# Performance work log

Measured on AMD Instinct MI355X. Metric: run time of the kernel, lower is better.

The kernel has to match this reference:

```python
import jax, jax.numpy as jnp
import numpy as np

B, T, C, H = 2, 2048, 1024, 16
D = C // H  # head dim = 64
EPS = 1e-5


def _layernorm(x, g, b):
    mu = jnp.mean(x, axis=-1, keepdims=True)
    var = jnp.mean((x - mu) ** 2, axis=-1, keepdims=True)
    return (x - mu) * jax.lax.rsqrt(var + EPS) * g + b


def setup_inputs() -> dict:
    key = jax.random.key(0)
    ks = jax.random.split(key, 16)
    s = 1.0 / np.sqrt(C)
    inp = {
        "x": jax.random.normal(ks[0], (B, T, C), dtype=jnp.float32),
        "Wq": jax.random.normal(ks[1], (C, C), dtype=jnp.float32) * s,
        "bq": jnp.zeros((C,), jnp.float32),
        "Wk": jax.random.normal(ks[2], (C, C), dtype=jnp.float32) * s,
        "bk": jnp.zeros((C,), jnp.float32),
        "Wv": jax.random.normal(ks[3], (C, C), dtype=jnp.float32) * s,
        "bv": jnp.zeros((C,), jnp.float32),
        "Wo": jax.random.normal(ks[4], (C, C), dtype=jnp.float32) * s,
        "bo": jnp.zeros((C,), jnp.float32),
        "ln1_g": jnp.ones((C,), jnp.float32),
        "ln1_b": jnp.zeros((C,), jnp.float32),
        "ln2_g": jnp.ones((C,), jnp.float32),
        "ln2_b": jnp.zeros((C,), jnp.float32),
        "W1": jax.random.normal(ks[5], (C, 4 * C), dtype=jnp.float32) * s,
        "b1": jnp.zeros((4 * C,), jnp.float32),
        "W2": jax.random.normal(ks[6], (4 * C, C), dtype=jnp.float32) * (1.0 / np.sqrt(4 * C)),
        "b2": jnp.zeros((C,), jnp.float32),
    }
    return inp


def _block(x, Wq, bq, Wk, bk, Wv, bv, Wo, bo, ln1_g, ln1_b, ln2_g, ln2_b, W1, b1, W2, b2):
    # --- attention sublayer (pre-LN, residual) ---
    h = _layernorm(x, ln1_g, ln1_b)
    q = (h @ Wq + bq).reshape(B, T, H, D)
    k = (h @ Wk + bk).reshape(B, T, H, D)
    v = (h @ Wv + bv).reshape(B, T, H, D)
    scores = jnp.einsum("bthd,bshd->bhts", q, k) * (1.0 / np.sqrt(D))
    attn = jax.nn.softmax(scores, axis=-1)  # dropout is identity at eval
    y = jnp.einsum("bhts,bshd->bthd", attn, v).reshape(B, T, C)
    x = x + (y @ Wo + bo)
    # --- MLP sublayer (pre-LN, residual) ---
    h2 = _layernorm(x, ln2_g, ln2_b)
    m = jax.nn.gelu(h2 @ W1 + b1, approximate=False)  # torch nn.GELU() is exact erf
    x = x + (m @ W2 + b2)
    return x


def reference(x, Wq, bq, Wk, bk, Wv, bv, Wo, bo, ln1_g, ln1_b, ln2_g, ln2_b, W1, b1, W2, b2):
    return _block(x, Wq, bq, Wk, bk, Wv, bv, Wo, bo, ln1_g, ln1_b, ln2_g, ln2_b, W1, b1, W2, b2)
```

## Files before the change

### kernel.cpp

```cpp
#include <hip/hip_runtime.h>
#include <math.h>

typedef unsigned short u16;
typedef unsigned int   u32;
using bf16x8 = __attribute__((ext_vector_type(8))) short;
using f32x4  = __attribute__((ext_vector_type(4))) float;
using f32x16 = __attribute__((ext_vector_type(16))) float;

static constexpr int Bb = 2, Tt = 2048, Cc = 1024, Hh = 16, Dd = 64;
static constexpr int QS = 3072;

__device__ __forceinline__ u16 f2bf(float f){
  u32 u = __builtin_bit_cast(u32, f);
  u += 0x7fffu + ((u >> 16) & 1u);
  return (u16)(u >> 16);
}

__device__ __forceinline__ void gl2lds16(const void* g, void* l){
  __builtin_amdgcn_global_load_lds((const __attribute__((address_space(1))) void*)g,
                                   (__attribute__((address_space(3))) void*)l, 16, 0, 0);
}

template<int N> __device__ __forceinline__ void waitvm(){
  if constexpr (N == 0) asm volatile("s_waitcnt vmcnt(0)" ::: "memory");
  else if constexpr (N == 3) asm volatile("s_waitcnt vmcnt(3)" ::: "memory");
  else if constexpr (N == 4) asm volatile("s_waitcnt vmcnt(4)" ::: "memory");
}

__device__ __forceinline__ void barrier_pin(){
  __builtin_amdgcn_s_barrier();
  __builtin_amdgcn_sched_barrier(0);
}

__device__ __forceinline__ f32x4 mfma16(bf16x8 a, bf16x8 b, f32x4 c){
  return __builtin_amdgcn_mfma_f32_16x16x32_bf16(a, b, c, 0, 0, 0);
}
__device__ __forceinline__ f32x16 mfma32(bf16x8 a, bf16x8 b, f32x16 c){
  return __builtin_amdgcn_mfma_f32_32x32x16_bf16(a, b, c, 0, 0, 0);
}

__device__ __forceinline__ float exp2f_fast(float x){
#if __has_builtin(__builtin_amdgcn_exp2f)
  return __builtin_amdgcn_exp2f(x);
#else
  return __expf(x * 0.69314718056f);
#endif
}

__device__ __forceinline__ float gelu_f(float x){
  return 0.5f * x * (1.0f + erff(x * 0.70710678118654752f));
}

__device__ __forceinline__ void plane_swap(u32& a, u32& b){
  asm("v_permlane32_swap_b32 %0, %1" : "+v"(a), "+v"(b));
}
__device__ __forceinline__ u32 cvtpk_bf16(float lo, float hi){
  u32 r;
  asm("v_cvt_pk_bf16_f32 %0, %1, %2" : "=v"(r) : "v"(lo), "v"(hi));
  return r;
}

__global__ __launch_bounds__(256) void ln_kernel(const float* __restrict__ x,
    const float* __restrict__ g, const float* __restrict__ b, u16* __restrict__ out)
{
  int row = blockIdx.x;
  int tid = threadIdx.x;
  const float4* xr = (const float4*)(x + (size_t)row * Cc);
  float4 v = xr[tid];
  float s  = v.x + v.y + v.z + v.w;
  float s2 = v.x*v.x + v.y*v.y + v.z*v.z + v.w*v.w;
  #pragma unroll
  for (int off = 1; off < 64; off <<= 1){ s += __shfl_xor(s, off); s2 += __shfl_xor(s2, off); }
  __shared__ float red[8];
  int wid = tid >> 6;
  if ((tid & 63) == 0){ red[wid] = s; red[4 + wid] = s2; }
  __syncthreads();
  s  = red[0] + red[1] + red[2] + red[3];
  s2 = red[4] + red[5] + red[6] + red[7];
  float mu   = s * (1.0f / Cc);
  float var  = s2 * (1.0f / Cc) - mu * mu;
  float rstd = rsqrtf(var + 1e-5f);
  const float4 gg = ((const float4*)g)[tid];
  const float4 bb = ((const float4*)b)[tid];
  ushort4 o;
  o.x = f2bf((v.x - mu) * rstd * gg.x + bb.x);
  o.y = f2bf((v.y - mu) * rstd * gg.y + bb.y);
  o.z = f2bf((v.z - mu) * rstd * gg.z + bb.z);
  o.w = f2bf((v.w - mu) * rstd * gg.w + bb.w);
  *(ushort4*)(out + (size_t)row * Cc + tid * 4) = o;
}

__global__ __launch_bounds__(256) void transpose_cast_kernel(const float* __restrict__ in,
    u16* __restrict__ out, int R, int Ccols)
{
  __shared__ float tile[32][33];
  int tx = threadIdx.x, ty = threadIdx.y;
  int c0 = blockIdx.x * 32, r0 = blockIdx.y * 32;
  #pragma unroll
  for (int j = 0; j < 4; j++) tile[ty + j*8][tx] = in[(size_t)(r0 + ty + j*8) * Ccols + c0 + tx];
  __syncthreads();
  #pragma unroll
  for (int j = 0; j < 4; j++) out[(size_t)(c0 + ty + j*8) * R + r0 + tx] = f2bf(tile[tx][ty + j*8]);
}

__global__ __launch_bounds__(256) void pack3_kernel(const float* __restrict__ a,
    const float* __restrict__ b, const float* __restrict__ c, float* __restrict__ o)
{
  int i = blockIdx.x * 256 + threadIdx.x;
  float v = (i < 1024) ? a[i] : (i < 2048 ? b[i - 1024] : c[i - 2048]);
  o[i] = v;
}

__global__ __launch_bounds__(256) void transpose_v_kernel(const u16* __restrict__ v, u16* __restrict__ vt)
{
  __shared__ u16 tile[32][33];
  int tx = threadIdx.x, ty = threadIdx.y;
  int bh = blockIdx.z; int b = bh >> 4, h = bh & 15;
  int t0 = blockIdx.x * 32, d0 = blockIdx.y * 32;
  const u16* src = v + (size_t)b * Tt * QS + h * Dd;
  #pragma unroll
  for (int j = 0; j < 4; j++) tile[ty + j*8][tx] = src[(size_t)(t0 + ty + j*8) * QS + d0 + tx];
  __syncthreads();
  u16* dst = vt + (size_t)bh * Dd * Tt;
  #pragma unroll
  for (int j = 0; j < 4; j++) dst[(size_t)(d0 + ty + j*8) * Tt + t0 + tx] = tile[tx][ty + j*8];
}

template<int BM, int BN, int EPI>
__global__ __launch_bounds__(256) void gemm_kernel(const u16* __restrict__ A, const u16* __restrict__ BT,
    const float* __restrict__ bias, const float* __restrict__ resid, void* __restrict__ out,
    int K, int ldA, int ldOut)
{
  constexpr int NLOADS = BM/64 + BN/64;
  constexpr int MI = BM/32, NI = BN/32;
  __shared__ alignas(16) u16 As[2][BM*32];
  __shared__ alignas(16) u16 Bs[2][BN*32];
  int tid  = threadIdx.x;
  int lane = tid & 63, wid = tid >> 6;
  int l15  = lane & 15, lg = lane >> 4;

  int gx = gridDim.x;
  int lin = blockIdx.x + gx * blockIdx.y;
  int nwg = gx * gridDim.y;
  int chunk = nwg >> 3;
  int wl = (lin & 7) * chunk + (lin >> 3);
  int rowBase = (wl % gx) * BM, colBase = (wl / gx) * BN;

  int wr = wid >> 1, wc = wid & 1;

  const u16* pA = A  + (size_t)(rowBase + (tid >> 2)) * ldA + ((tid & 3) << 3);
  const u16* pB = BT + (size_t)(colBase + (tid >> 2)) * K   + ((tid & 3) << 3);

  f32x4 acc[MI][NI] = {};

  auto stage = [&](int buf, int k0){
    #pragma unroll
    for (int j = 0; j < BM/64; j++)
      gl2lds16(pA + (size_t)j * 64 * ldA + k0, (u16*)As[buf] + j * 2048 + wid * 512);
    #pragma unroll
    for (int j = 0; j < BN/64; j++)
      gl2lds16(pB + (size_t)j * 64 * K + k0, (u16*)Bs[buf] + j * 2048 + wid * 512);
  };

  stage(0, 0);
  int cur = 0;
  for (int k0 = 0; k0 < K; k0 += 32) {
    if (k0 + 32 < K) { stage(cur ^ 1, k0 + 32); waitvm<NLOADS>(); }
    else             { waitvm<0>(); }
    barrier_pin();

    bf16x8 a[MI], b[NI];
    #pragma unroll
    for (int i = 0; i < MI; i++)
      a[i] = *(const bf16x8*)((u16*)As[cur] + (wr * (BM/2) + i * 16 + l15) * 32 + lg * 8);
    #pragma unroll
    for (int i = 0; i < NI; i++)
      b[i] = *(const bf16x8*)((u16*)Bs[cur] + (wc * (BN/2) + i * 16 + l15) * 32 + lg * 8);
    #pragma unroll
    for (int mi = 0; mi < MI; mi++)
      #pragma unroll
      for (int ni = 0; ni < NI; ni++)
        acc[mi][ni] = mfma16(a[mi], b[ni], acc[mi][ni]);

    __builtin_amdgcn_sched_barrier(0);
    barrier_pin();
    cur ^= 1;
  }

  #pragma unroll
  for (int mi = 0; mi < MI; mi++){
    #pragma unroll
    for (int ni = 0; ni < NI; ni++){
      int row = rowBase + wr * (BM/2) + mi * 16 + lg * 4;
      int col = colBase + wc * (BN/2) + ni * 16 + l15;
      float bc = bias[col];
      #pragma unroll
      for (int r = 0; r < 4; r++){
        float val = acc[mi][ni][r] + bc;
        size_t idx = (size_t)(row + r) * ldOut + col;
        if constexpr (EPI == 0)      ((u16*)out)[idx]   = f2bf(val);
        else if constexpr (EPI == 1) ((float*)out)[idx] = val + resid[idx];
        else                         ((u16*)out)[idx]   = f2bf(gelu_f(val));
      }
    }
  }
}

__global__ __launch_bounds__(256) void attn_kernel(const u16* __restrict__ q, const u16* __restrict__ k,
    const u16* __restrict__ vt, u16* __restrict__ y)
{
  __shared__ alignas(16) u16 Ks[2][64 * 64];
  __shared__ alignas(16) u16 Vs[2][64 * 64];
  int tid  = threadIdx.x;
  int lane = tid & 63, wid = tid >> 6;
  int l31  = lane & 31, hi = lane >> 5;

  int lin = blockIdx.x + 16 * blockIdx.y;
  int wl  = (lin & 7) * 64 + (lin >> 3);
  int qt  = wl & 15, bh = wl >> 4;
  int b = bh >> 4, h = bh & 15;

  int qglob = qt * 128 + wid * 32 + l31;

  const u16* qp = q + ((size_t)b * Tt + qglob) * QS + h * Dd + hi * 8;
  bf16x8 qf[4];
  #pragma unroll
  for (int s = 0; s < 4; s++) qf[s] = *(const bf16x8*)(qp + s * 16);

  const u16* kbase = k  + (size_t)b * Tt * QS + h * Dd;
  const u16* vbase = vt + (size_t)bh * Dd * Tt;

  f32x16 yacc[2] = {};
  float m2 = -1e30f, lsum = 0.f;
  const float CL = 0.125f * 1.44269504089f;

  int g0 = tid, g1 = tid + 256;
  int r0 = g0 >> 3, cb0 = (g0 & 7) ^ (r0 & 7);
  int r1 = g1 >> 3, cb1 = (g1 & 7) ^ (r1 & 7);

  auto stageKV = [&](int buf, int kt){
    gl2lds16(kbase + (size_t)(kt + r0) * QS + cb0 * 8, (u16*)Ks[buf] + wid * 512);
    gl2lds16(kbase + (size_t)(kt + r1) * QS + cb1 * 8, (u16*)Ks[buf] + 2048 + wid * 512);
    gl2lds16(vbase + (size_t)r0 * Tt + kt + cb0 * 8,   (u16*)Vs[buf] + wid * 512);
    gl2lds16(vbase + (size_t)r1 * Tt + kt + cb1 * 8,   (u16*)Vs[buf] + 2048 + wid * 512);
  };

  stageKV(0, 0);
  int cur = 0;
  for (int kt = 0; kt < Tt; kt += 64) {
    if (kt + 64 < Tt) { stageKV(cur ^ 1, kt + 64); waitvm<4>(); }
    else              { waitvm<0>(); }
    barrier_pin();

    const u16* Ksb = (const u16*)Ks[cur];
    const u16* Vsb = (const u16*)Vs[cur];
    int rx = l31 & 7;

    f32x16 st[2] = {};
    __builtin_amdgcn_s_setprio(1);
    #pragma unroll
    for (int nb = 0; nb < 2; nb++){
      const u16* krow = Ksb + (nb * 32 + l31) * 64;
      #pragma unroll
      for (int s = 0; s < 4; s++){
        bf16x8 kf = *(const bf16x8*)(krow + (((s * 2 + hi) ^ rx) << 3));
        st[nb] = mfma32(kf, qf[s], st[nb]);
      }
    }
    __builtin_amdgcn_s_setprio(0);

    float tm[16];
    #pragma unroll
    for (int i = 0; i < 16; i++) tm[i] = fmaxf(st[0][i], st[1][i]);
    #pragma unroll
    for (int w = 8; w; w >>= 1)
      #pragma unroll
      for (int i = 0; i < w; i++) tm[i] = fmaxf(tm[i], tm[i + w]);
    u32 ma = __builtin_bit_cast(u32, tm[0]), mb = ma;
    plane_swap(ma, mb);
    float mx = fmaxf(__builtin_bit_cast(float, ma), __builtin_bit_cast(float, mb));
    float mnew = fmaxf(m2, mx * CL);
    float alpha = exp2f_fast(m2 - mnew);
    m2 = mnew;

    #pragma unroll
    for (int nb = 0; nb < 2; nb++)
      #pragma unroll
      for (int i = 0; i < 16; i++)
        st[nb][i] = exp2f_fast(st[nb][i] * CL - mnew);

    float ts[16];
    #pragma unroll
    for (int i = 0; i < 16; i++) ts[i] = st[0][i] + st[1][i];
    #pragma unroll
    for (int w = 8; w; w >>= 1)
      #pragma unroll
      for (int i = 0; i < w; i++) ts[i] += ts[i + w];
    u32 sa = __builtin_bit_cast(u32, ts[0]), sb = sa;
    plane_swap(sa, sb);
    float rs = __builtin_bit_cast(float, sa) + __builtin_bit_cast(float, sb);
    lsum = lsum * alpha + rs;

    #pragma unroll
    for (int nd = 0; nd < 2; nd++)
      #pragma unroll
      for (int i = 0; i < 16; i++) yacc[nd][i] *= alpha;

    bf16x8 pb[4];
    #pragma unroll
    for (int nb = 0; nb < 2; nb++){
      u32 c[8];
      #pragma unroll
      for (int i = 0; i < 8; i++) c[i] = cvtpk_bf16(st[nb][2 * i], st[nb][2 * i + 1]);
      plane_swap(c[0], c[2]); plane_swap(c[1], c[3]);
      plane_swap(c[4], c[6]); plane_swap(c[5], c[7]);
      u32 f0[4] = {c[0], c[1], c[2], c[3]};
      u32 f1[4] = {c[4], c[5], c[6], c[7]};
      pb[nb * 2 + 0] = __builtin_bit_cast(bf16x8, *(const u32*)nullptr == 0 ? *(bf16x8*)f0 : *(bf16x8*)f0);
      pb[nb * 2 + 0] = *(bf16x8*)f0;
      pb[nb * 2 + 1] = *(bf16x8*)f1;
    }

    __builtin_amdgcn_s_setprio(1);
    #pragma unroll
    for (int nd = 0; nd < 2; nd++){
      const u16* vrow = Vsb + (nd * 32 + l31) * 64;
      #pragma unroll
      for (int ks = 0; ks < 4; ks++){
        bf16x8 vf = *(const bf16x8*)(vrow + (((ks * 2 + hi) ^ rx) << 3));
        yacc[nd] = mfma32(vf, pb[ks], yacc[nd]);
      }
    }
    __builtin_amdgcn_s_setprio(0);

    __builtin_amdgcn_sched_barrier(0);
    barrier_pin();
    cur ^= 1;
  }

  float inv = 1.0f / lsum;
  u16* yp = y + ((size_t)b * Tt + qt * 128 + wid * 32 + l31) * Cc + h * Dd;
  #pragma unroll
  for (int nd = 0; nd < 2; nd++){
    #pragma unroll
    for (int g = 0; g < 4; g++){
      ushort4 o;
      o.x = f2bf(yacc[nd][g * 4 + 0] * inv);
      o.y = f2bf(yacc[nd][g * 4 + 1] * inv);
      o.z = f2bf(yacc[nd][g * 4 + 2] * inv);
      o.w = f2bf(yacc[nd][g * 4 + 3] * inv);
      *(ushort4*)(yp + nd * 32 + g * 8 + hi * 4) = o;
    }
  }
}

extern "C" void kernel_launch(void* const* d_in, const int* in_sizes, int n_in,
                              void* d_out, int out_size, void* d_ws, size_t ws_size,
                              hipStream_t stream)
{
  (void)in_sizes; (void)n_in; (void)out_size; (void)ws_size;
  const float* x    = (const float*)d_in[0];
  const float* Wq   = (const float*)d_in[1];
  const float* bq   = (const float*)d_in[2];
  const float* Wk   = (const float*)d_in[3];
  const float* bk   = (const float*)d_in[4];
  const float* Wv   = (const float*)d_in[5];
  const float* bv   = (const float*)d_in[6];
  const float* Wo   = (const float*)d_in[7];
  const float* bo   = (const float*)d_in[8];
  const float* ln1g = (const float*)d_in[9];
  const float* ln1b = (const float*)d_in[10];
  const float* ln2g = (const float*)d_in[11];
  const float* ln2b = (const float*)d_in[12];
  const float* W1   = (const float*)d_in[13];
  const float* b1   = (const float*)d_in[14];
  const float* W2   = (const float*)d_in[15];
  const float* b2   = (const float*)d_in[16];

  char* ws = (char*)d_ws;
  const size_t MB = 1024 * 1024;
  u16*   wqkvt = (u16*)(ws + 0 * MB);
  u16*   wot   = (u16*)(ws + 6 * MB);
  u16*   w1t   = (u16*)(ws + 8 * MB);
  u16*   w2t   = (u16*)(ws + 16 * MB);
  float* bqkv  = (float*)(ws + 24 * MB);
  u16*   hbuf  = (u16*)(ws + 25 * MB);
  u16*   qkv   = (u16*)(ws + 33 * MB);
  u16*   vtb   = (u16*)(ws + 57 * MB);
  u16*   yb    = (u16*)(ws + 65 * MB);
  float* x2    = (float*)(ws + 73 * MB);
  u16*   h2    = hbuf;
  u16*   mb    = qkv;

  dim3 tb(32, 8);
  transpose_cast_kernel<<<dim3(32, 32),  tb, 0, stream>>>(Wq, wqkvt,                1024, 1024);
  transpose_cast_kernel<<<dim3(32, 32),  tb, 0, stream>>>(Wk, wqkvt + 1024 * 1024,  1024, 1024);
  transpose_cast_kernel<<<dim3(32, 32),  tb, 0, stream>>>(Wv, wqkvt + 2048 * 1024,  1024, 1024);
  transpose_cast_kernel<<<dim3(32, 32),  tb, 0, stream>>>(Wo, wot, 1024, 1024);
  transpose_cast_kernel<<<dim3(128, 32), tb, 0, stream>>>(W1, w1t, 1024, 4096);
  transpose_cast_kernel<<<dim3(32, 128), tb, 0, stream>>>(W2, w2t, 4096, 1024);
  pack3_kernel<<<12, 256, 0, stream>>>(bq, bk, bv, bqkv);

  ln_kernel<<<4096, 256, 0, stream>>>(x, ln1g, ln1b, hbuf);

  gemm_kernel<128, 128, 0><<<dim3(32, 24), 256, 0, stream>>>(hbuf, wqkvt, bqkv, nullptr, qkv, 1024, 1024, 3072);

  transpose_v_kernel<<<dim3(64, 2, 32), tb, 0, stream>>>(qkv + 2048, vtb);

  attn_kernel<<<dim3(16, 32), 256, 0, stream>>>(qkv, qkv + 1024, vtb, yb);

  gemm_kernel<64, 128, 1><<<dim3(64, 8), 256, 0, stream>>>(yb, wot, bo, x, x2, 1024, 1024, 1024);

  ln_kernel<<<4096, 256, 0, stream>>>(x2, ln2g, ln2b, h2);

  gemm_kernel<128, 128, 2><<<dim3(32, 32), 256, 0, stream>>>(h2, w1t, b1, nullptr, mb, 1024, 1024, 4096);

  gemm_kernel<64, 128, 1><<<dim3(64, 8), 256, 0, stream>>>(mb, w2t, b2, x2, (float*)d_out, 4096, 4096, 1024);
}
```

Measured before the change: 299.4 us.

## Rewrite GEMMs as 8-wave kernels with larger tiles, K=64 stages and swizzled LDS

Replaces the 4-wave GEMM with an 8-wave (512-thread) kernel that uses 256x256 or 128x128 tiles, a K-step of 64 and an XOR-swizzled LDS layout. The next tile's global-to-LDS loads are split into four phases and interleaved with the MFMA work, and MFMA sections run at raised wave priority. This aims to raise data reuse per LDS load, avoid LDS bank conflicts and hide load latency. The trade-off is much more LDS and fewer workgroups: the 256x256 QKV GEMM launches 192 blocks, which may under-fill the GPU. A dead null-pointer expression in the attention kernel is also removed.

Measured after the change: 354.2 us. +18.3%, slower.

```diff
diff --git a/kernel.cpp b/kernel.cpp
--- a/kernel.cpp
+++ b/kernel.cpp
@@ -23,7 +23,6 @@
 
 template<int N> __device__ __forceinline__ void waitvm(){
   if constexpr (N == 0) asm volatile("s_waitcnt vmcnt(0)" ::: "memory");
-  else if constexpr (N == 3) asm volatile("s_waitcnt vmcnt(3)" ::: "memory");
   else if constexpr (N == 4) asm volatile("s_waitcnt vmcnt(4)" ::: "memory");
 }
 
@@ -127,72 +126,107 @@
 }
 
 template<int BM, int BN, int EPI>
-__global__ __launch_bounds__(256) void gemm_kernel(const u16* __restrict__ A, const u16* __restrict__ BT,
+__global__ __launch_bounds__(512, 2) void gemm8_kernel(const u16* __restrict__ A, const u16* __restrict__ BT,
     const float* __restrict__ bias, const float* __restrict__ resid, void* __restrict__ out,
     int K, int ldA, int ldOut)
 {
-  constexpr int NLOADS = BM/64 + BN/64;
-  constexpr int MI = BM/32, NI = BN/32;
-  __shared__ alignas(16) u16 As[2][BM*32];
-  __shared__ alignas(16) u16 Bs[2][BN*32];
+  constexpr int MF = BM / 32;
+  constexpr int NF = BN / 64;
+  constexpr int AG = BM / 64;
+  constexpr int BG = BN / 64;
+  constexpr int LT = AG + BG;
+  constexpr int LPP = LT / 4;
+
+  __shared__ alignas(16) u16 As[2][BM * 64];
+  __shared__ alignas(16) u16 Bs[2][BN * 64];
+
   int tid  = threadIdx.x;
   int lane = tid & 63, wid = tid >> 6;
   int l15  = lane & 15, lg = lane >> 4;
 
-  int gx = gridDim.x;
+  int gx  = gridDim.x;
   int lin = blockIdx.x + gx * blockIdx.y;
   int nwg = gx * gridDim.y;
-  int chunk = nwg >> 3;
-  int wl = (lin & 7) * chunk + (lin >> 3);
+  int wl  = (lin & 7) * (nwg >> 3) + (lin >> 3);
   int rowBase = (wl % gx) * BM, colBase = (wl / gx) * BN;
 
-  int wr = wid >> 1, wc = wid & 1;
-
-  const u16* pA = A  + (size_t)(rowBase + (tid >> 2)) * ldA + ((tid & 3) << 3);
-  const u16* pB = BT + (size_t)(colBase + (tid >> 2)) * K   + ((tid & 3) << 3);
-
-  f32x4 acc[MI][NI] = {};
-
-  auto stage = [&](int buf, int k0){
-    #pragma unroll
-    for (int j = 0; j < BM/64; j++)
-      gl2lds16(pA + (size_t)j * 64 * ldA + k0, (u16*)As[buf] + j * 2048 + wid * 512);
-    #pragma unroll
-    for (int j = 0; j < BN/64; j++)
-      gl2lds16(pB + (size_t)j * 64 * K + k0, (u16*)Bs[buf] + j * 2048 + wid * 512);
-  };
-
-  stage(0, 0);
+  int wr = wid >> 2, wc = wid & 3;
+
+  f32x4 acc[MF][NF] = {};
+
+  #pragma unroll
+  for (int j = 0; j < AG; j++){
+    int g = tid + 512 * j;
+    gl2lds16(A + (size_t)(rowBase + (g >> 3)) * ldA + (((g & 7) ^ ((g >> 3) & 7)) << 3),
+             (u16*)As[0] + g * 8);
+  }
+  #pragma unroll
+  for (int j = 0; j < BG; j++){
+    int g = tid + 512 * j;
+    gl2lds16(BT + (size_t)(colBase + (g >> 3)) * K + (((g & 7) ^ ((g >> 3) & 7)) << 3),
+             (u16*)Bs[0] + g * 8);
+  }
+
   int cur = 0;
-  for (int k0 = 0; k0 < K; k0 += 32) {
-    if (k0 + 32 < K) { stage(cur ^ 1, k0 + 32); waitvm<NLOADS>(); }
-    else             { waitvm<0>(); }
-    barrier_pin();
-
-    bf16x8 a[MI], b[NI];
-    #pragma unroll
-    for (int i = 0; i < MI; i++)
-      a[i] = *(const bf16x8*)((u16*)As[cur] + (wr * (BM/2) + i * 16 + l15) * 32 + lg * 8);
-    #pragma unroll
-    for (int i = 0; i < NI; i++)
-      b[i] = *(const bf16x8*)((u16*)Bs[cur] + (wc * (BN/2) + i * 16 + l15) * 32 + lg * 8);
-    #pragma unroll
-    for (int mi = 0; mi < MI; mi++)
-      #pragma unroll
-      for (int ni = 0; ni < NI; ni++)
-        acc[mi][ni] = mfma16(a[mi], b[ni], acc[mi][ni]);
-
-    __builtin_amdgcn_sched_barrier(0);
-    barrier_pin();
-    cur ^= 1;
-  }
-
-  #pragma unroll
-  for (int mi = 0; mi < MI; mi++){
-    #pragma unroll
-    for (int ni = 0; ni < NI; ni++){
-      int row = rowBase + wr * (BM/2) + mi * 16 + lg * 4;
-      int col = colBase + wc * (BN/2) + ni * 16 + l15;
+  for (int k0 = 0; k0 < K; k0 += 64, cur ^= 1){
+    __syncthreads();
+    const u16* Asb = (const u16*)As[cur];
+    const u16* Bsb = (const u16*)Bs[cur];
+    const bool more = (k0 + 64 < K);
+    const int kn = k0 + 64;
+
+    #pragma unroll
+    for (int p = 0; p < 4; p++){
+      if (more){
+        #pragma unroll
+        for (int j = p * LPP; j < (p + 1) * LPP; j++){
+          if (j < AG){
+            int g = tid + 512 * j;
+            gl2lds16(A + (size_t)(rowBase + (g >> 3)) * ldA + kn + (((g & 7) ^ ((g >> 3) & 7)) << 3),
+                     (u16*)As[cur ^ 1] + g * 8);
+          } else {
+            int g = tid + 512 * (j - AG);
+            gl2lds16(BT + (size_t)(colBase + (g >> 3)) * K + kn + (((g & 7) ^ ((g >> 3) & 7)) << 3),
+                     (u16*)Bs[cur ^ 1] + g * 8);
+          }
+        }
+      }
+
+      int pm = p >> 1, pn = p & 1;
+      bf16x8 a[MF / 2][2], b[NF / 2][2];
+      #pragma unroll
+      for (int mi = 0; mi < MF / 2; mi++){
+        int r = wr * (BM / 2) + (pm * (MF / 2) + mi) * 16 + l15;
+        #pragma unroll
+        for (int kh = 0; kh < 2; kh++)
+          a[mi][kh] = *(const bf16x8*)(Asb + r * 64 + (((kh * 4 + lg) ^ (r & 7)) << 3));
+      }
+      #pragma unroll
+      for (int ni = 0; ni < NF / 2; ni++){
+        int r = wc * (BN / 4) + (pn * (NF / 2) + ni) * 16 + l15;
+        #pragma unroll
+        for (int kh = 0; kh < 2; kh++)
+          b[ni][kh] = *(const bf16x8*)(Bsb + r * 64 + (((kh * 4 + lg) ^ (r & 7)) << 3));
+      }
+      __builtin_amdgcn_s_setprio(1);
+      #pragma unroll
+      for (int mi = 0; mi < MF / 2; mi++)
+        #pragma unroll
+        for (int ni = 0; ni < NF / 2; ni++)
+          #pragma unroll
+          for (int kh = 0; kh < 2; kh++)
+            acc[pm * (MF / 2) + mi][pn * (NF / 2) + ni] =
+                mfma16(a[mi][kh], b[ni][kh], acc[pm * (MF / 2) + mi][pn * (NF / 2) + ni]);
+      __builtin_amdgcn_s_setprio(0);
+    }
+  }
+
+  #pragma unroll
+  for (int mi = 0; mi < MF; mi++){
+    #pragma unroll
+    for (int ni = 0; ni < NF; ni++){
+      int row = rowBase + wr * (BM / 2) + mi * 16 + lg * 4;
+      int col = colBase + wc * (BN / 4) + ni * 16 + l15;
       float bc = bias[col];
       #pragma unroll
       for (int r = 0; r < 4; r++){
@@ -316,7 +350,6 @@
       plane_swap(c[4], c[6]); plane_swap(c[5], c[7]);
       u32 f0[4] = {c[0], c[1], c[2], c[3]};
       u32 f1[4] = {c[4], c[5], c[6], c[7]};
-      pb[nb * 2 + 0] = __builtin_bit_cast(bf16x8, *(const u32*)nullptr == 0 ? *(bf16x8*)f0 : *(bf16x8*)f0);
       pb[nb * 2 + 0] = *(bf16x8*)f0;
       pb[nb * 2 + 1] = *(bf16x8*)f1;
     }
@@ -403,17 +436,17 @@
 
   ln_kernel<<<4096, 256, 0, stream>>>(x, ln1g, ln1b, hbuf);
 
-  gemm_kernel<128, 128, 0><<<dim3(32, 24), 256, 0, stream>>>(hbuf, wqkvt, bqkv, nullptr, qkv, 1024, 1024, 3072);
+  gemm8_kernel<256, 256, 0><<<dim3(16, 12), 512, 0, stream>>>(hbuf, wqkvt, bqkv, nullptr, qkv, 1024, 1024, 3072);
 
   transpose_v_kernel<<<dim3(64, 2, 32), tb, 0, stream>>>(qkv + 2048, vtb);
 
   attn_kernel<<<dim3(16, 32), 256, 0, stream>>>(qkv, qkv + 1024, vtb, yb);
 
-  gemm_kernel<64, 128, 1><<<dim3(64, 8), 256, 0, stream>>>(yb, wot, bo, x, x2, 1024, 1024, 1024);
+  gemm8_kernel<128, 128, 1><<<dim3(32, 8), 512, 0, stream>>>(yb, wot, bo, x, x2, 1024, 1024, 1024);
 
   ln_kernel<<<4096, 256, 0, stream>>>(x2, ln2g, ln2b, h2);
 
-  gemm_kernel<128, 128, 2><<<dim3(32, 32), 256, 0, stream>>>(h2, w1t, b1, nullptr, mb, 1024, 1024, 4096);
-
-  gemm_kernel<64, 128, 1><<<dim3(64, 8), 256, 0, stream>>>(mb, w2t, b2, x2, (float*)d_out, 4096, 4096, 1024);
-}
+  gemm8_kernel<256, 256, 2><<<dim3(16, 16), 512, 0, stream>>>(h2, w1t, b1, nullptr, mb, 1024, 1024, 4096);
+
+  gemm8_kernel<128, 128, 1><<<dim3(32, 8), 512, 0, stream>>>(mb, w2t, b2, x2, (float*)d_out, 4096, 4096, 1024);
+}
```

## Rework GEMM with larger tiles, K=64 steps, XOR-swizzled LDS and merged weight transposes

Applied to the files above, without the earlier changes.

Replaces the GEMM with a configurable kernel that stages 64-wide K slices into XOR-swizzled shared memory, uses larger block tiles (256x256 with 8 waves for QKV and W1, 128x128 for the output projections) and raises MFMA priority during compute. The swizzle is meant to avoid LDS bank conflicts, and the bigger tiles and K step are meant to improve data reuse and cut per-iteration barrier overhead. It drops the grouped workgroup remapping, and the large tiles launch far fewer blocks (192 and 256), which may underfill the GPU's compute units. It also merges the four square weight transposes into one launch and removes a stray null-pointer dereference line in the attention kernel.

After: 280.4 us. 6.4% less time.

```diff
diff --git a/kernel.cpp b/kernel.cpp
--- a/kernel.cpp
+++ b/kernel.cpp
@@ -23,8 +23,8 @@
 
 template<int N> __device__ __forceinline__ void waitvm(){
   if constexpr (N == 0) asm volatile("s_waitcnt vmcnt(0)" ::: "memory");
-  else if constexpr (N == 3) asm volatile("s_waitcnt vmcnt(3)" ::: "memory");
   else if constexpr (N == 4) asm volatile("s_waitcnt vmcnt(4)" ::: "memory");
+  else if constexpr (N == 8) asm volatile("s_waitcnt vmcnt(8)" ::: "memory");
 }
 
 __device__ __forceinline__ void barrier_pin(){
@@ -103,6 +103,24 @@
   for (int j = 0; j < 4; j++) out[(size_t)(c0 + ty + j*8) * R + r0 + tx] = f2bf(tile[tx][ty + j*8]);
 }
 
+__global__ __launch_bounds__(256) void transpose4_kernel(
+    const float* __restrict__ s0, const float* __restrict__ s1,
+    const float* __restrict__ s2, const float* __restrict__ s3,
+    u16* __restrict__ d0, u16* __restrict__ d1, u16* __restrict__ d2, u16* __restrict__ d3)
+{
+  __shared__ float tile[32][33];
+  int z = blockIdx.z;
+  const float* in = (z == 0) ? s0 : (z == 1) ? s1 : (z == 2) ? s2 : s3;
+  u16* out        = (z == 0) ? d0 : (z == 1) ? d1 : (z == 2) ? d2 : d3;
+  int tx = threadIdx.x, ty = threadIdx.y;
+  int c0 = blockIdx.x * 32, r0 = blockIdx.y * 32;
+  #pragma unroll
+  for (int j = 0; j < 4; j++) tile[ty + j*8][tx] = in[(size_t)(r0 + ty + j*8) * 1024 + c0 + tx];
+  __syncthreads();
+  #pragma unroll
+  for (int j = 0; j < 4; j++) out[(size_t)(c0 + ty + j*8) * 1024 + r0 + tx] = f2bf(tile[tx][ty + j*8]);
+}
+
 __global__ __launch_bounds__(256) void pack3_kernel(const float* __restrict__ a,
     const float* __restrict__ b, const float* __restrict__ c, float* __restrict__ o)
 {
@@ -126,73 +144,89 @@
   for (int j = 0; j < 4; j++) dst[(size_t)(d0 + ty + j*8) * Tt + t0 + tx] = tile[tx][ty + j*8];
 }
 
-template<int BM, int BN, int EPI>
-__global__ __launch_bounds__(256) void gemm_kernel(const u16* __restrict__ A, const u16* __restrict__ BT,
-    const float* __restrict__ bias, const float* __restrict__ resid, void* __restrict__ out,
-    int K, int ldA, int ldOut)
-{
-  constexpr int NLOADS = BM/64 + BN/64;
-  constexpr int MI = BM/32, NI = BN/32;
-  __shared__ alignas(16) u16 As[2][BM*32];
-  __shared__ alignas(16) u16 Bs[2][BN*32];
-  int tid  = threadIdx.x;
-  int lane = tid & 63, wid = tid >> 6;
-  int l15  = lane & 15, lg = lane >> 4;
-
-  int gx = gridDim.x;
-  int lin = blockIdx.x + gx * blockIdx.y;
-  int nwg = gx * gridDim.y;
-  int chunk = nwg >> 3;
-  int wl = (lin & 7) * chunk + (lin >> 3);
-  int rowBase = (wl % gx) * BM, colBase = (wl / gx) * BN;
-
-  int wr = wid >> 1, wc = wid & 1;
-
-  const u16* pA = A  + (size_t)(rowBase + (tid >> 2)) * ldA + ((tid & 3) << 3);
-  const u16* pB = BT + (size_t)(colBase + (tid >> 2)) * K   + ((tid & 3) << 3);
-
-  f32x4 acc[MI][NI] = {};
+template<int BM, int BN, int WM, int WN, int EPI>
+__global__ __launch_bounds__(WM * WN * 64, 2) void gemmc_kernel(
+    const u16* __restrict__ A, const u16* __restrict__ BT,
+    const float* __restrict__ bias, const float* __restrict__ resid,
+    void* __restrict__ out, int K, int ldA, int ldOut)
+{
+  constexpr int THREADS = WM * WN * 64;
+  constexpr int MF = (BM / WM) / 16;
+  constexpr int NF = (BN / WN) / 16;
+  constexpr int AG = (BM * 8) / THREADS;
+  constexpr int BG = (BN * 8) / THREADS;
+
+  __shared__ alignas(16) u16 As[2][BM * 64];
+  __shared__ alignas(16) u16 Bs[2][BN * 64];
+
+  const int tid  = threadIdx.x;
+  const int lane = tid & 63, wid = tid >> 6;
+  const int l15  = lane & 15, lg = lane >> 4;
+  const int rowBase = blockIdx.x * BM, colBase = blockIdx.y * BN;
+  const int wr = wid / WN, wc = wid % WN;
+
+  f32x4 acc[MF][NF] = {};
 
   auto stage = [&](int buf, int k0){
     #pragma unroll
-    for (int j = 0; j < BM/64; j++)
-      gl2lds16(pA + (size_t)j * 64 * ldA + k0, (u16*)As[buf] + j * 2048 + wid * 512);
-    #pragma unroll
-    for (int j = 0; j < BN/64; j++)
-      gl2lds16(pB + (size_t)j * 64 * K + k0, (u16*)Bs[buf] + j * 2048 + wid * 512);
+    for (int j = 0; j < AG; j++){
+      int g = tid + THREADS * j;
+      int row = g >> 3, ch = (g & 7) ^ (row & 7);
+      gl2lds16(A + (size_t)(rowBase + row) * ldA + k0 + ch * 8,
+               (u16*)As[buf] + (wid * 64 + THREADS * j) * 8);
+    }
+    #pragma unroll
+    for (int j = 0; j < BG; j++){
+      int g = tid + THREADS * j;
+      int row = g >> 3, ch = (g & 7) ^ (row & 7);
+      gl2lds16(BT + (size_t)(colBase + row) * K + k0 + ch * 8,
+               (u16*)Bs[buf] + (wid * 64 + THREADS * j) * 8);
+    }
   };
 
   stage(0, 0);
+  const int nt = K >> 6;
   int cur = 0;
-  for (int k0 = 0; k0 < K; k0 += 32) {
-    if (k0 + 32 < K) { stage(cur ^ 1, k0 + 32); waitvm<NLOADS>(); }
-    else             { waitvm<0>(); }
-    barrier_pin();
-
-    bf16x8 a[MI], b[NI];
-    #pragma unroll
-    for (int i = 0; i < MI; i++)
-      a[i] = *(const bf16x8*)((u16*)As[cur] + (wr * (BM/2) + i * 16 + l15) * 32 + lg * 8);
-    #pragma unroll
-    for (int i = 0; i < NI; i++)
-      b[i] = *(const bf16x8*)((u16*)Bs[cur] + (wc * (BN/2) + i * 16 + l15) * 32 + lg * 8);
-    #pragma unroll
-    for (int mi = 0; mi < MI; mi++)
-      #pragma unroll
-      for (int ni = 0; ni < NI; ni++)
-        acc[mi][ni] = mfma16(a[mi], b[ni], acc[mi][ni]);
-
+  for (int t = 0; t < nt; ++t, cur ^= 1){
+    if (t + 1 < nt){ stage(cur ^ 1, (t + 1) << 6); waitvm<8>(); }
+    else           { waitvm<0>(); }
+    __builtin_amdgcn_s_barrier();
     __builtin_amdgcn_sched_barrier(0);
-    barrier_pin();
-    cur ^= 1;
+
+    const u16* Asb = (const u16*)As[cur];
+    const u16* Bsb = (const u16*)Bs[cur];
+
+    bf16x8 bfr[NF][2];
+    #pragma unroll
+    for (int ni = 0; ni < NF; ni++){
+      int r = wc * (BN / WN) + ni * 16 + l15;
+      bfr[ni][0] = *(const bf16x8*)(Bsb + r * 64 + ((lg       ^ (r & 7)) << 3));
+      bfr[ni][1] = *(const bf16x8*)(Bsb + r * 64 + (((4 + lg) ^ (r & 7)) << 3));
+    }
+    #pragma unroll
+    for (int mi = 0; mi < MF; mi++){
+      int r = wr * (BM / WM) + mi * 16 + l15;
+      bf16x8 a0 = *(const bf16x8*)(Asb + r * 64 + ((lg       ^ (r & 7)) << 3));
+      bf16x8 a1 = *(const bf16x8*)(Asb + r * 64 + (((4 + lg) ^ (r & 7)) << 3));
+      __builtin_amdgcn_s_setprio(1);
+      #pragma unroll
+      for (int ni = 0; ni < NF; ni++){
+        acc[mi][ni] = mfma16(a0, bfr[ni][0], acc[mi][ni]);
+        acc[mi][ni] = mfma16(a1, bfr[ni][1], acc[mi][ni]);
+      }
+      __builtin_amdgcn_s_setprio(0);
+    }
+
+    __builtin_amdgcn_sched_barrier(0);
+    __builtin_amdgcn_s_barrier();
   }
 
   #pragma unroll
-  for (int mi = 0; mi < MI; mi++){
-    #pragma unroll
-    for (int ni = 0; ni < NI; ni++){
-      int row = rowBase + wr * (BM/2) + mi * 16 + lg * 4;
-      int col = colBase + wc * (BN/2) + ni * 16 + l15;
+  for (int mi = 0; mi < MF; mi++){
+    #pragma unroll
+    for (int ni = 0; ni < NF; ni++){
+      int row = rowBase + wr * (BM / WM) + mi * 16 + lg * 4;
+      int col = colBase + wc * (BN / WN) + ni * 16 + l15;
       float bc = bias[col];
       #pragma unroll
       for (int r = 0; r < 4; r++){
@@ -316,7 +350,6 @@
       plane_swap(c[4], c[6]); plane_swap(c[5], c[7]);
       u32 f0[4] = {c[0], c[1], c[2], c[3]};
       u32 f1[4] = {c[4], c[5], c[6], c[7]};
-      pb[nb * 2 + 0] = __builtin_bit_cast(bf16x8, *(const u32*)nullptr == 0 ? *(bf16x8*)f0 : *(bf16x8*)f0);
       pb[nb * 2 + 0] = *(bf16x8*)f0;
       pb[nb * 2 + 1] = *(bf16x8*)f1;
     }
@@ -393,27 +426,25 @@
   u16*   mb    = qkv;
 
   dim3 tb(32, 8);
-  transpose_cast_kernel<<<dim3(32, 32),  tb, 0, stream>>>(Wq, wqkvt,                1024, 1024);
-  transpose_cast_kernel<<<dim3(32, 32),  tb, 0, stream>>>(Wk, wqkvt + 1024 * 1024,  1024, 1024);
-  transpose_cast_kernel<<<dim3(32, 32),  tb, 0, stream>>>(Wv, wqkvt + 2048 * 1024,  1024, 1024);
-  transpose_cast_kernel<<<dim3(32, 32),  tb, 0, stream>>>(Wo, wot, 1024, 1024);
+  transpose4_kernel<<<dim3(32, 32, 4), tb, 0, stream>>>(Wq, Wk, Wv, Wo,
+      wqkvt, wqkvt + 1024 * 1024, wqkvt + 2048 * 1024, wot);
   transpose_cast_kernel<<<dim3(128, 32), tb, 0, stream>>>(W1, w1t, 1024, 4096);
   transpose_cast_kernel<<<dim3(32, 128), tb, 0, stream>>>(W2, w2t, 4096, 1024);
   pack3_kernel<<<12, 256, 0, stream>>>(bq, bk, bv, bqkv);
 
   ln_kernel<<<4096, 256, 0, stream>>>(x, ln1g, ln1b, hbuf);
 
-  gemm_kernel<128, 128, 0><<<dim3(32, 24), 256, 0, stream>>>(hbuf, wqkvt, bqkv, nullptr, qkv, 1024, 1024, 3072);
+  gemmc_kernel<256, 256, 2, 4, 0><<<dim3(16, 12), 512, 0, stream>>>(hbuf, wqkvt, bqkv, nullptr, qkv, 1024, 1024, 3072);
 
   transpose_v_kernel<<<dim3(64, 2, 32), tb, 0, stream>>>(qkv + 2048, vtb);
 
   attn_kernel<<<dim3(16, 32), 256, 0, stream>>>(qkv, qkv + 1024, vtb, yb);
 
-  gemm_kernel<64, 128, 1><<<dim3(64, 8), 256, 0, stream>>>(yb, wot, bo, x, x2, 1024, 1024, 1024);
+  gemmc_kernel<128, 128, 2, 2, 1><<<dim3(32, 8), 256, 0, stream>>>(yb, wot, bo, x, x2, 1024, 1024, 1024);
 
   ln_kernel<<<4096, 256, 0, stream>>>(x2, ln2g, ln2b, h2);
 
-  gemm_kernel<128, 128, 2><<<dim3(32, 32), 256, 0, stream>>>(h2, w1t, b1, nullptr, mb, 1024, 1024, 4096);
-
-  gemm_kernel<64, 128, 1><<<dim3(64, 8), 256, 0, stream>>>(mb, w2t, b2, x2, (float*)d_out, 4096, 4096, 1024);
-}
+  gemmc_kernel<256, 256, 2, 4, 2><<<dim3(16, 16), 512, 0, stream>>>(h2, w1t, b1, nullptr, mb, 1024, 1024, 4096);
+
+  gemmc_kernel<128, 128, 2, 2, 1><<<dim3(32, 8), 256, 0, stream>>>(mb, w2t, b2, x2, (float*)d_out, 4096, 4096, 1024);
+}
```
